# Optimization experiments

Hardware: AMD Instinct MI355X
Metric: run time of the kernel (lower is better)

## Reference

```python
import jax, jax.numpy as jnp
import numpy as np

HIDDEN = 2048
N_HEADS = 16
N_KV_HEADS = 4
HEAD_DIM = 128
N_REP = N_HEADS // N_KV_HEADS
BATCH = 2
SEQ = 2048
SCALE = HEAD_DIM ** -0.5
NEG = -1e9


def apply_rope(x, freqs):
    # x: (b, s, h, d); freqs: (s, d//2) angles. Interleaved-pair rotation.
    cos = jnp.cos(freqs)[None, :, None, :]
    sin = jnp.sin(freqs)[None, :, None, :]
    x1 = x[..., 0::2]
    x2 = x[..., 1::2]
    r1 = x1 * cos - x2 * sin
    r2 = x1 * sin + x2 * cos
    return jnp.stack([r1, r2], axis=-1).reshape(x.shape)


def setup_inputs() -> dict:
    key = jax.random.key(0)
    ks = jax.random.split(key, 6)
    x = jax.random.normal(ks[0], (BATCH, SEQ, HIDDEN), dtype=jnp.float32)
    wq = jax.random.normal(ks[1], (N_HEADS * HEAD_DIM, HIDDEN), dtype=jnp.float32) * 0.02
    wk = jax.random.normal(ks[2], (N_KV_HEADS * HEAD_DIM, HIDDEN), dtype=jnp.float32) * 0.02
    wv = jax.random.normal(ks[3], (N_KV_HEADS * HEAD_DIM, HIDDEN), dtype=jnp.float32) * 0.02
    wo = jax.random.normal(ks[4], (HIDDEN, N_HEADS * HEAD_DIM), dtype=jnp.float32) * 0.02
    # RoPE angle table: pos * theta^{-2i/d}
    inv_freq = 1.0 / (10000.0 ** (jnp.arange(0, HEAD_DIM, 2, dtype=jnp.float32) / HEAD_DIM))
    rope_freqs = jnp.arange(SEQ, dtype=jnp.float32)[:, None] * inv_freq[None, :]  # (S, d/2)
    # additive causal mask
    causal = jnp.tril(jnp.ones((SEQ, SEQ), dtype=bool))
    mask = jnp.where(causal, 0.0, NEG).astype(jnp.float32)[None, None]  # (1,1,S,S)
    return {"x": x, "wq": wq, "wk": wk, "wv": wv, "wo": wo,
            "rope_freqs": rope_freqs, "mask": mask}


def reference(x, wq, wk, wv, wo, rope_freqs, mask):
    b, s, _ = x.shape
    q = (x @ wq.T).reshape(b, s, N_HEADS, HEAD_DIM)
    k = (x @ wk.T).reshape(b, s, N_KV_HEADS, HEAD_DIM)
    v = (x @ wv.T).reshape(b, s, N_KV_HEADS, HEAD_DIM)
    q = apply_rope(q, rope_freqs)
    k = apply_rope(k, rope_freqs)
    new_k, new_v = k, v  # kv cache (no prior cache, start_pos=0)
    # GQA: repeat each kv head n_rep times (matches expand+reshape in source)
    k_rep = jnp.repeat(k, N_REP, axis=2)  # (b, s, n_heads, d)
    v_rep = jnp.repeat(v, N_REP, axis=2)
    scores = jnp.einsum('bqhd,bkhd->bhqk', q, k_rep) * SCALE
    scores = scores + mask
    attn = jax.nn.softmax(scores.astype(jnp.float32), axis=-1).astype(q.dtype)
    out = jnp.einsum('bhqk,bkhd->bqhd', attn, v_rep).reshape(b, s, -1)
    return out @ wo.T, (new_k, new_v)
```

## Files before the change

kernel.cpp:

```cpp
#include <hip/hip_runtime.h>
#include <hip/hip_bf16.h>

#define NH 16
#define NKV 4
#define HD 128
#define QSCALE 0.1275174272f

using bf16x8 = __attribute__((ext_vector_type(8))) __bf16;
using f32x4  = __attribute__((ext_vector_type(4))) float;
using u16x8  = __attribute__((ext_vector_type(8))) unsigned short;
using u16x2  = __attribute__((ext_vector_type(2))) unsigned short;

__device__ __forceinline__ unsigned short f2b(float f) {
  __hip_bfloat16 h = __float2bfloat16(f);
  return __builtin_bit_cast(unsigned short, h);
}
__device__ __forceinline__ float b2f(unsigned short u) {
  unsigned int v = ((unsigned int)u) << 16;
  return __builtin_bit_cast(float, v);
}

__device__ __forceinline__ void glds16(const unsigned short* g, unsigned short* l) {
  __builtin_amdgcn_global_load_lds(
      (const __attribute__((address_space(1))) unsigned int*)(const void*)g,
      (__attribute__((address_space(3))) unsigned int*)(void*)l, 16, 0, 0);
}

__global__ __launch_bounds__(256) void cvt_fused(const float* __restrict__ x,
                                                 const float* __restrict__ wq,
                                                 const float* __restrict__ wk,
                                                 const float* __restrict__ wv,
                                                 const float* __restrict__ wo,
                                                 unsigned short* __restrict__ xb,
                                                 unsigned short* __restrict__ wqkvb,
                                                 unsigned short* __restrict__ wob) {
  int i = blockIdx.x * 256 + threadIdx.x;
  const float* src;
  unsigned short* dst;
  int off;
  if (i < 1048576)      { src = x;  dst = xb;              off = i; }
  else if (i < 1572864) { src = wq; dst = wqkvb;           off = i - 1048576; }
  else if (i < 1703936) { src = wk; dst = wqkvb + 4194304; off = i - 1572864; }
  else if (i < 1835008) { src = wv; dst = wqkvb + 5242880; off = i - 1703936; }
  else                  { src = wo; dst = wob;             off = i - 1835008; }
  const float4* s4 = reinterpret_cast<const float4*>(src) + (size_t)off * 2;
  float4 v0 = s4[0], v1 = s4[1];
  u16x8 o;
  o[0] = f2b(v0.x); o[1] = f2b(v0.y); o[2] = f2b(v0.z); o[3] = f2b(v0.w);
  o[4] = f2b(v1.x); o[5] = f2b(v1.y); o[6] = f2b(v1.z); o[7] = f2b(v1.w);
  reinterpret_cast<u16x8*>(dst)[off] = o;
}

template<int CF32, int WROWS>
__global__ __launch_bounds__(256, 2) void gemm_p(const unsigned short* __restrict__ A,
                                                 const unsigned short* __restrict__ B,
                                                 void* __restrict__ C,
                                                 int N, int K, int nbx) {
  constexpr int AF  = WROWS / 16;
  constexpr int AL  = WROWS / 32;
  constexpr int ACH = WROWS * 8;
  __shared__ unsigned short As[3][ACH * 8];
  __shared__ unsigned short Bs[3][4096];
  const int tid = threadIdx.x, lane = tid & 63, wid = tid >> 6;
  const int wm = wid >> 1, wn = wid & 1;
  const int cpx = gridDim.x >> 3;
  const int wgid = (blockIdx.x & 7) * cpx + (blockIdx.x >> 3);
  const int bx = wgid % nbx, by = wgid / nbx;
  const int row0 = by * (2 * WROWS), col0 = bx * 128;
  const int fr = lane & 15, g = lane >> 4;
  const int NT = K >> 5;

  size_t offA[AL], offB[2];
#pragma unroll
  for (int l = 0; l < AL; l++) {
    int cid = tid + l * 256;
    int R = cid >> 3, p = cid & 7, cl = p ^ (R & 7);
    offA[l] = (size_t)(row0 + 2 * R + (cl >> 2)) * K + (cl & 3) * 8;
  }
#pragma unroll
  for (int l = 0; l < 2; l++) {
    int cid = tid + l * 256;
    int R = cid >> 3, p = cid & 7, cl = p ^ (R & 7);
    offB[l] = (size_t)(col0 + 2 * R + (cl >> 2)) * K + (cl & 3) * 8;
  }

  auto stage = [&](int t, int sb) {
    int k0 = t * 32;
#pragma unroll
    for (int l = 0; l < AL; l++)
      glds16(A + offA[l] + k0, &As[sb][tid * 8 + l * 2048]);
#pragma unroll
    for (int l = 0; l < 2; l++)
      glds16(B + offB[l] + k0, &Bs[sb][tid * 8 + l * 2048]);
  };

  f32x4 acc[AF][4];
#pragma unroll
  for (int i = 0; i < AF; i++)
#pragma unroll
    for (int j = 0; j < 4; j++) acc[i][j] = f32x4{0.f, 0.f, 0.f, 0.f};

  stage(0, 0);
  stage(1, 1);
  if constexpr (WROWS == 128)
    asm volatile("s_waitcnt vmcnt(6)" ::: "memory");
  else
    asm volatile("s_waitcnt vmcnt(4)" ::: "memory");
  __builtin_amdgcn_s_barrier();
  asm volatile("" ::: "memory");

  const int cp8 = ((((fr & 1) << 2) | g) ^ ((fr >> 1) & 7)) * 8;
  const int rr = fr >> 1;

  int rb = 0, sb = 2;
#pragma unroll 1
  for (int t = 0; t < NT; ++t) {
    if (t + 2 < NT) stage(t + 2, sb);

    bf16x8 af[AF], bfr[4];
#pragma unroll
    for (int i = 0; i < AF; i++)
      af[i] = *reinterpret_cast<const bf16x8*>(&As[rb][(wm * (WROWS / 2) + i * 8 + rr) * 64 + cp8]);
#pragma unroll
    for (int j = 0; j < 4; j++)
      bfr[j] = *reinterpret_cast<const bf16x8*>(&Bs[rb][(wn * 32 + j * 8 + rr) * 64 + cp8]);

    __builtin_amdgcn_s_setprio(1);
#pragma unroll
    for (int i = 0; i < AF; i++)
#pragma unroll
      for (int j = 0; j < 4; j++)
        acc[i][j] = __builtin_amdgcn_mfma_f32_16x16x32_bf16(af[i], bfr[j], acc[i][j], 0, 0, 0);
    __builtin_amdgcn_s_setprio(0);

    if (t + 1 < NT) {
      if (t + 2 < NT) {
        if constexpr (WROWS == 128)
          asm volatile("s_waitcnt vmcnt(6)" ::: "memory");
        else
          asm volatile("s_waitcnt vmcnt(4)" ::: "memory");
      } else {
        asm volatile("s_waitcnt vmcnt(0)" ::: "memory");
      }
      __builtin_amdgcn_s_barrier();
      asm volatile("" ::: "memory");
    }
    rb = rb == 2 ? 0 : rb + 1;
    sb = sb == 2 ? 0 : sb + 1;
  }

  const int r4 = g * 4;
#pragma unroll
  for (int i = 0; i < AF; i++) {
#pragma unroll
    for (int j = 0; j < 4; j++) {
      int rbase = row0 + wm * WROWS + i * 16 + r4;
      int cb = col0 + wn * 64 + j * 16 + fr;
#pragma unroll
      for (int r = 0; r < 4; r++) {
        if (CF32)
          reinterpret_cast<float*>(C)[(size_t)(rbase + r) * N + cb] = acc[i][j][r];
        else
          reinterpret_cast<unsigned short*>(C)[(size_t)(rbase + r) * N + cb] = f2b(acc[i][j][r]);
      }
    }
  }
}

__global__ __launch_bounds__(256) void rope_kernel(const unsigned short* __restrict__ qkv,
                                                   const float* __restrict__ freqs,
                                                   unsigned short* __restrict__ qro,
                                                   unsigned short* __restrict__ kro,
                                                   float* __restrict__ newk) {
  const int NQ = 4096 * 16 * 64;
  const int NK = 4096 * 4 * 64;
  int idx = blockIdx.x * 256 + threadIdx.x;
  if (idx >= NQ + NK) return;
  if (idx < NQ) {
    int i = idx & 63;
    int h = (idx >> 6) & 15;
    int row = idx >> 10;
    int s = row & 2047, b = row >> 11;
    float f = freqs[s * 64 + i];
    float c = cosf(f), sn = sinf(f);
    u16x2 xv = *reinterpret_cast<const u16x2*>(qkv + (size_t)row * 3072 + h * 128 + 2 * i);
    float x1 = b2f(xv.x), x2 = b2f(xv.y);
    float r1 = (x1 * c - x2 * sn) * QSCALE;
    float r2 = (x1 * sn + x2 * c) * QSCALE;
    u16x2 o; o.x = f2b(r1); o.y = f2b(r2);
    *reinterpret_cast<u16x2*>(qro + ((size_t)(b * 16 + h) * 2048 + s) * 128 + 2 * i) = o;
  } else {
    idx -= NQ;
    int i = idx & 63;
    int h = (idx >> 6) & 3;
    int row = idx >> 8;
    int s = row & 2047, b = row >> 11;
    float f = freqs[s * 64 + i];
    float c = cosf(f), sn = sinf(f);
    u16x2 xv = *reinterpret_cast<const u16x2*>(qkv + (size_t)row * 3072 + 2048 + h * 128 + 2 * i);
    float x1 = b2f(xv.x), x2 = b2f(xv.y);
    float r1 = x1 * c - x2 * sn;
    float r2 = x1 * sn + x2 * c;
    u16x2 o; o.x = f2b(r1); o.y = f2b(r2);
    *reinterpret_cast<u16x2*>(kro + ((size_t)(b * 4 + h) * 2048 + s) * 128 + 2 * i) = o;
    float2 of; of.x = r1; of.y = r2;
    *reinterpret_cast<float2*>(newk + (size_t)row * 512 + h * 128 + 2 * i) = of;
  }
}

__global__ __launch_bounds__(256) void vtrans_kernel(const unsigned short* __restrict__ qkv,
                                                     unsigned short* __restrict__ vt,
                                                     float* __restrict__ newv) {
  __shared__ unsigned short T[32][136];
  const int st = blockIdx.x;
  const int kvh = blockIdx.y & 3, b = blockIdx.y >> 2;
  const int s0 = st * 32;
  const int t = threadIdx.x;
  const int ls = t >> 3;
  const int ch = (t & 7) * 2;
  const unsigned short* src = qkv + (size_t)(b * 2048 + s0 + ls) * 3072 + 2560 + kvh * 128 + ch * 8;
  u16x8 a0 = *reinterpret_cast<const u16x8*>(src);
  u16x8 a1 = *reinterpret_cast<const u16x8*>(src + 8);
  *reinterpret_cast<u16x8*>(&T[ls][ch * 8])     = a0;
  *reinterpret_cast<u16x8*>(&T[ls][ch * 8 + 8]) = a1;
  float* nv = newv + (size_t)(b * 2048 + s0 + ls) * 512 + kvh * 128 + ch * 8;
  float4 f0, f1, f2, f3;
  f0.x = b2f(a0[0]); f0.y = b2f(a0[1]); f0.z = b2f(a0[2]); f0.w = b2f(a0[3]);
  f1.x = b2f(a0[4]); f1.y = b2f(a0[5]); f1.z = b2f(a0[6]); f1.w = b2f(a0[7]);
  f2.x = b2f(a1[0]); f2.y = b2f(a1[1]); f2.z = b2f(a1[2]); f2.w = b2f(a1[3]);
  f3.x = b2f(a1[4]); f3.y = b2f(a1[5]); f3.z = b2f(a1[6]); f3.w = b2f(a1[7]);
  reinterpret_cast<float4*>(nv)[0] = f0;
  reinterpret_cast<float4*>(nv)[1] = f1;
  reinterpret_cast<float4*>(nv)[2] = f2;
  reinterpret_cast<float4*>(nv)[3] = f3;
  __syncthreads();
  const int d = t >> 1, half = t & 1;
  unsigned short* dst = vt + ((size_t)(b * 4 + kvh) * 128 + d) * 2048 + s0 + half * 16;
  u16x8 o0, o1;
#pragma unroll
  for (int q = 0; q < 8; q++) {
    int slot = half * 16 + q;
    int kl = ((slot >> 2) & 1) * 16 + (slot >> 3) * 4 + (slot & 3);
    o0[q] = T[kl][d];
  }
#pragma unroll
  for (int q = 0; q < 8; q++) {
    int slot = half * 16 + 8 + q;
    int kl = ((slot >> 2) & 1) * 16 + (slot >> 3) * 4 + (slot & 3);
    o1[q] = T[kl][d];
  }
  reinterpret_cast<u16x8*>(dst)[0] = o0;
  reinterpret_cast<u16x8*>(dst)[1] = o1;
}

__global__ __launch_bounds__(256, 4) void attn_kernel(const unsigned short* __restrict__ qro,
                                                      const unsigned short* __restrict__ kro,
                                                      const unsigned short* __restrict__ vt,
                                                      unsigned short* __restrict__ out) {
  __shared__ unsigned short Ks[2][32 * 128];
  __shared__ unsigned short Vs[2][64 * 64];
  const int tid = threadIdx.x, lane = tid & 63, w = tid >> 6;
  const int kvhb = blockIdx.x & 7;
  const int kvh = kvhb & 3, b = kvhb >> 2;
  const int t = 127 - (blockIdx.x >> 3);
  const int h = kvh * 4 + w;
  const int qbase = t * 16;
  const int fr = lane & 15, g = lane >> 4, fk = g * 8;
  const unsigned short* Kp = kro + (size_t)(b * 4 + kvh) * 2048 * 128;
  const unsigned short* Vtp = vt + (size_t)(b * 4 + kvh) * 128 * 2048;
  const unsigned short* Qp = qro + ((size_t)(b * 16 + h) * 2048 + qbase) * 128;

  bf16x8 qf[4];
#pragma unroll
  for (int kk = 0; kk < 4; kk++)
    qf[kk] = *reinterpret_cast<const bf16x8*>(Qp + fr * 128 + kk * 32 + fk);

  u16x8 onesu;
#pragma unroll
  for (int j = 0; j < 8; j++) onesu[j] = 0x3F80;
  bf16x8 ones = __builtin_bit_cast(bf16x8, onesu);

  f32x4 o[8];
#pragma unroll
  for (int dt = 0; dt < 8; dt++) o[dt] = f32x4{0.f, 0.f, 0.f, 0.f};
  f32x4 dacc = f32x4{0.f, 0.f, 0.f, 0.f};
  const int qrow_s = qbase + fr;
  const int nfull = (qbase >= 31) ? ((qbase - 31) >> 5) + 1 : 0;
  const int niter = nfull + 1;

  const int krow = w * 8 + (lane >> 4);
  const int kcol = lane & 15;
  const int vrow = w * 16 + (lane >> 3);
  const int vcol = lane & 7;

  auto stage = [&](int kv0, int buf) {
    unsigned short* Kb = &Ks[buf][0];
    unsigned short* Vb = &Vs[buf][0];
#pragma unroll
    for (int j = 0; j < 2; j++) {
      int r = krow + j * 4;
      glds16(Kp + (size_t)(kv0 + r) * 128 + ((kcol ^ (r & 7)) * 8),
             Kb + (w * 8 + j * 4) * 128);
    }
#pragma unroll
    for (int j = 0; j < 2; j++) {
      int r = vrow + j * 8;
      int u = vcol ^ (r & 7);
      int d = 2 * r + (u >> 2);
      glds16(Vtp + (size_t)d * 2048 + kv0 + (u & 3) * 8,
             Vb + (w * 16 + j * 8) * 64);
    }
  };

  auto step = [&](int kv0, bool mask, int buf) {
    const unsigned short* Kb = &Ks[buf][0];
    const unsigned short* Vb = &Vs[buf][0];
    f32x4 sc[2];
    sc[0] = sc[1] = f32x4{0.f, 0.f, 0.f, 0.f};
    __builtin_amdgcn_s_setprio(1);
#pragma unroll
    for (int kk = 0; kk < 4; kk++) {
      int blk = ((kk * 4 + g) ^ (fr & 7)) * 8;
      bf16x8 ka0 = *reinterpret_cast<const bf16x8*>(Kb + (fr +  0) * 128 + blk);
      bf16x8 ka1 = *reinterpret_cast<const bf16x8*>(Kb + (fr + 16) * 128 + blk);
      sc[0] = __builtin_amdgcn_mfma_f32_16x16x32_bf16(ka0, qf[kk], sc[0], 0, 0, 0);
      sc[1] = __builtin_amdgcn_mfma_f32_16x16x32_bf16(ka1, qf[kk], sc[1], 0, 0, 0);
    }
    __builtin_amdgcn_s_setprio(0);
#pragma unroll
    for (int s = 0; s < 2; s++)
#pragma unroll
      for (int r = 0; r < 4; r++) {
        float v = sc[s][r];
        if (mask && (kv0 + 16 * s + 4 * g + r > qrow_s)) v = -1e30f;
        sc[s][r] = __builtin_amdgcn_exp2f(v);
      }
    u16x8 pau;
#pragma unroll
    for (int j = 0; j < 4; j++) {
      pau[j]     = f2b(sc[0][j]);
      pau[4 + j] = f2b(sc[1][j]);
    }
    bf16x8 pa = __builtin_bit_cast(bf16x8, pau);
    dacc = __builtin_amdgcn_mfma_f32_16x16x32_bf16(pa, ones, dacc, 0, 0, 0);
    __builtin_amdgcn_s_setprio(1);
#pragma unroll
    for (int dt = 0; dt < 8; dt++) {
      int jr = dt * 8 + (fr >> 1);
      int c = ((fr & 1) * 4 + g) ^ (fr >> 1);
      bf16x8 vf = *reinterpret_cast<const bf16x8*>(Vb + jr * 64 + c * 8);
      o[dt] = __builtin_amdgcn_mfma_f32_16x16x32_bf16(pa, vf, o[dt], 0, 0, 0);
    }
    __builtin_amdgcn_s_setprio(0);
  };

  stage(0, 0);
  int buf = 0;
  for (int i = 0; i < niter; i++) {
    __syncthreads();
    if (i + 1 < niter) stage((i + 1) * 32, buf ^ 1);
    step(i * 32, i == nfull, buf);
    buf ^= 1;
  }

#pragma unroll
  for (int r = 0; r < 4; r++) {
    float inv = 1.0f / dacc[r];
    int qrow = qbase + g * 4 + r;
    size_t rowoff = ((size_t)b * 2048 + qrow) * 2048 + (size_t)h * 128;
#pragma unroll
    for (int dt = 0; dt < 8; dt++)
      out[rowoff + dt * 16 + fr] = f2b(o[dt][r] * inv);
  }
}

extern "C" void kernel_launch(void* const* d_in, const int* in_sizes, int n_in,
                              void* d_out, int out_size, void* d_ws, size_t ws_size,
                              hipStream_t stream) {
  const float* x  = (const float*)d_in[0];
  const float* wq = (const float*)d_in[1];
  const float* wk = (const float*)d_in[2];
  const float* wv = (const float*)d_in[3];
  const float* wo = (const float*)d_in[4];
  const float* freqs = (const float*)d_in[5];

  char* ws = (char*)d_ws;
  unsigned short* xb    = (unsigned short*)(ws);
  unsigned short* attn  = xb;
  unsigned short* wqkvb = (unsigned short*)(ws + 16777216);
  unsigned short* wob   = (unsigned short*)(ws + 29360128);
  unsigned short* qkv   = (unsigned short*)(ws + 37748736);
  unsigned short* qro   = (unsigned short*)(ws + 62914560);
  unsigned short* kro   = (unsigned short*)(ws + 79691776);
  unsigned short* vt    = (unsigned short*)(ws + 83886080);

  float* out_o = (float*)d_out;
  float* out_k = (float*)d_out + 8388608;
  float* out_v = (float*)d_out + 10485760;

  cvt_fused<<<9216, 256, 0, stream>>>(x, wq, wk, wv, wo, xb, wqkvb, wob);

  gemm_p<0, 128><<<384, 256, 0, stream>>>(xb, wqkvb, qkv, 3072, 2048, 24);

  rope_kernel<<<20480, 256, 0, stream>>>(qkv, freqs, qro, kro, out_k);
  vtrans_kernel<<<dim3(64, 8), 256, 0, stream>>>(qkv, vt, out_v);

  attn_kernel<<<1024, 256, 0, stream>>>(qro, kro, vt, attn);

  gemm_p<1, 64><<<512, 256, 0, stream>>>(attn, wob, out_o, 2048, 2048, 16);
}
```

Baseline: 216.5 us.

## Replace GEMM with 8-wave 128x256 tile kernel using split-phase staging

Swaps the 4-wave GEMM for an 8-wave, 512-thread kernel with 128x256 output tiles and a K-step of 64. Each iteration is split into two halves, and the global-to-LDS staging for a future tile is interleaved with the MFMA work through explicit barriers and sched_barriers. The aim is more operand reuse per tile and better overlap of memory traffic with matrix math. In exchange it uses more LDS and registers, allows one block per CU, and leaves fewer blocks for the output projection (256), which risks lower occupancy and tail effects.

```diff
diff --git a/kernel.cpp b/kernel.cpp
--- a/kernel.cpp
+++ b/kernel.cpp
@@ -51,110 +51,127 @@
   reinterpret_cast<u16x8*>(dst)[off] = o;
 }
 
-template<int CF32, int WROWS>
-__global__ __launch_bounds__(256, 2) void gemm_p(const unsigned short* __restrict__ A,
-                                                 const unsigned short* __restrict__ B,
-                                                 void* __restrict__ C,
-                                                 int N, int K, int nbx) {
-  constexpr int AF  = WROWS / 16;
-  constexpr int AL  = WROWS / 32;
-  constexpr int ACH = WROWS * 8;
-  __shared__ unsigned short As[3][ACH * 8];
-  __shared__ unsigned short Bs[3][4096];
-  const int tid = threadIdx.x, lane = tid & 63, wid = tid >> 6;
-  const int wm = wid >> 1, wn = wid & 1;
+template<int CF32>
+__global__ __launch_bounds__(512, 1) void gemm8(const unsigned short* __restrict__ A,
+                                                const unsigned short* __restrict__ B,
+                                                void* __restrict__ C,
+                                                int N, int K, int nbx) {
+  __shared__ unsigned short As[3][128 * 64];
+  __shared__ unsigned short Bs[3][256 * 64];
+  const int tid = threadIdx.x, lane = tid & 63;
+  const int wid = tid >> 6, wm = wid >> 2, wn = wid & 3;
   const int cpx = gridDim.x >> 3;
   const int wgid = (blockIdx.x & 7) * cpx + (blockIdx.x >> 3);
   const int bx = wgid % nbx, by = wgid / nbx;
-  const int row0 = by * (2 * WROWS), col0 = bx * 128;
+  const int row0 = by * 128, col0 = bx * 256;
   const int fr = lane & 15, g = lane >> 4;
-  const int NT = K >> 5;
-
-  size_t offA[AL], offB[2];
-#pragma unroll
-  for (int l = 0; l < AL; l++) {
-    int cid = tid + l * 256;
-    int R = cid >> 3, p = cid & 7, cl = p ^ (R & 7);
-    offA[l] = (size_t)(row0 + 2 * R + (cl >> 2)) * K + (cl & 3) * 8;
-  }
+  const int NT = K >> 6;
+
+  size_t offA[2], offB[4];
 #pragma unroll
   for (int l = 0; l < 2; l++) {
-    int cid = tid + l * 256;
-    int R = cid >> 3, p = cid & 7, cl = p ^ (R & 7);
-    offB[l] = (size_t)(col0 + 2 * R + (cl >> 2)) * K + (cl & 3) * 8;
-  }
-
-  auto stage = [&](int t, int sb) {
-    int k0 = t * 32;
-#pragma unroll
-    for (int l = 0; l < AL; l++)
-      glds16(A + offA[l] + k0, &As[sb][tid * 8 + l * 2048]);
-#pragma unroll
-    for (int l = 0; l < 2; l++)
-      glds16(B + offB[l] + k0, &Bs[sb][tid * 8 + l * 2048]);
-  };
-
-  f32x4 acc[AF][4];
-#pragma unroll
-  for (int i = 0; i < AF; i++)
+    int cid = tid + l * 512, R = cid >> 3, phys = cid & 7, cl = phys ^ (R & 7);
+    offA[l] = (size_t)(row0 + R) * K + cl * 8;
+  }
+#pragma unroll
+  for (int l = 0; l < 4; l++) {
+    int cid = tid + l * 512, R = cid >> 3, phys = cid & 7, cl = phys ^ (R & 7);
+    offB[l] = (size_t)(col0 + R) * K + cl * 8;
+  }
+
+  auto stage0 = [&](int t, int sb) {
+    int k0 = t * 64;
+    glds16(A + offA[0] + k0, &As[sb][tid * 8]);
+    glds16(A + offA[1] + k0, &As[sb][(tid + 512) * 8]);
+    glds16(B + offB[0] + k0, &Bs[sb][tid * 8]);
+  };
+  auto stage1 = [&](int t, int sb) {
+    int k0 = t * 64;
+    glds16(B + offB[1] + k0, &Bs[sb][(tid + 512) * 8]);
+    glds16(B + offB[2] + k0, &Bs[sb][(tid + 1024) * 8]);
+    glds16(B + offB[3] + k0, &Bs[sb][(tid + 1536) * 8]);
+  };
+
+  const int ca = fr & 7;
+  auto ldA = [&](int rb, int mf, int ks) {
+    return *reinterpret_cast<const bf16x8*>(
+        &As[rb][(wm * 64 + mf * 16 + fr) * 64 + (((ks << 2) | g) ^ ca) * 8]);
+  };
+  auto ldB = [&](int rb, int nf, int ks) {
+    return *reinterpret_cast<const bf16x8*>(
+        &Bs[rb][(wn * 64 + nf * 16 + fr) * 64 + (((ks << 2) | g) ^ ca) * 8]);
+  };
+
+  f32x4 acc[4][4];
+#pragma unroll
+  for (int i = 0; i < 4; i++)
 #pragma unroll
     for (int j = 0; j < 4; j++) acc[i][j] = f32x4{0.f, 0.f, 0.f, 0.f};
 
-  stage(0, 0);
-  stage(1, 1);
-  if constexpr (WROWS == 128)
-    asm volatile("s_waitcnt vmcnt(6)" ::: "memory");
-  else
-    asm volatile("s_waitcnt vmcnt(4)" ::: "memory");
+  stage0(0, 0); stage1(0, 0);
+  stage0(1, 1); stage1(1, 1);
+  asm volatile("s_waitcnt vmcnt(6)" ::: "memory");
   __builtin_amdgcn_s_barrier();
-  asm volatile("" ::: "memory");
-
-  const int cp8 = ((((fr & 1) << 2) | g) ^ ((fr >> 1) & 7)) * 8;
-  const int rr = fr >> 1;
+  __builtin_amdgcn_sched_barrier(0);
 
   int rb = 0, sb = 2;
 #pragma unroll 1
   for (int t = 0; t < NT; ++t) {
-    if (t + 2 < NT) stage(t + 2, sb);
-
-    bf16x8 af[AF], bfr[4];
-#pragma unroll
-    for (int i = 0; i < AF; i++)
-      af[i] = *reinterpret_cast<const bf16x8*>(&As[rb][(wm * (WROWS / 2) + i * 8 + rr) * 64 + cp8]);
-#pragma unroll
-    for (int j = 0; j < 4; j++)
-      bfr[j] = *reinterpret_cast<const bf16x8*>(&Bs[rb][(wn * 32 + j * 8 + rr) * 64 + cp8]);
-
+    bf16x8 bfr[4][2];
+#pragma unroll
+    for (int nf = 0; nf < 4; nf++) { bfr[nf][0] = ldB(rb, nf, 0); bfr[nf][1] = ldB(rb, nf, 1); }
+    bf16x8 a0[2][2];
+#pragma unroll
+    for (int mf = 0; mf < 2; mf++) { a0[mf][0] = ldA(rb, mf, 0); a0[mf][1] = ldA(rb, mf, 1); }
+    if (t + 2 < NT) stage0(t + 2, sb);
+    __builtin_amdgcn_s_barrier();
+    asm volatile("s_waitcnt lgkmcnt(0)" ::: "memory");
+    __builtin_amdgcn_sched_barrier(0);
     __builtin_amdgcn_s_setprio(1);
 #pragma unroll
-    for (int i = 0; i < AF; i++)
-#pragma unroll
-      for (int j = 0; j < 4; j++)
-        acc[i][j] = __builtin_amdgcn_mfma_f32_16x16x32_bf16(af[i], bfr[j], acc[i][j], 0, 0, 0);
+    for (int mf = 0; mf < 2; mf++)
+#pragma unroll
+      for (int nf = 0; nf < 4; nf++) {
+        acc[mf][nf] = __builtin_amdgcn_mfma_f32_16x16x32_bf16(a0[mf][0], bfr[nf][0], acc[mf][nf], 0, 0, 0);
+        acc[mf][nf] = __builtin_amdgcn_mfma_f32_16x16x32_bf16(a0[mf][1], bfr[nf][1], acc[mf][nf], 0, 0, 0);
+      }
     __builtin_amdgcn_s_setprio(0);
+    __builtin_amdgcn_sched_barrier(0);
+    __builtin_amdgcn_s_barrier();
+
+    bf16x8 a1[2][2];
+#pragma unroll
+    for (int mf = 0; mf < 2; mf++) { a1[mf][0] = ldA(rb, mf + 2, 0); a1[mf][1] = ldA(rb, mf + 2, 1); }
+    if (t + 2 < NT) stage1(t + 2, sb);
+    __builtin_amdgcn_s_barrier();
+    asm volatile("s_waitcnt lgkmcnt(0)" ::: "memory");
+    __builtin_amdgcn_sched_barrier(0);
+    __builtin_amdgcn_s_setprio(1);
+#pragma unroll
+    for (int mf = 0; mf < 2; mf++)
+#pragma unroll
+      for (int nf = 0; nf < 4; nf++) {
+        acc[mf + 2][nf] = __builtin_amdgcn_mfma_f32_16x16x32_bf16(a1[mf][0], bfr[nf][0], acc[mf + 2][nf], 0, 0, 0);
+        acc[mf + 2][nf] = __builtin_amdgcn_mfma_f32_16x16x32_bf16(a1[mf][1], bfr[nf][1], acc[mf + 2][nf], 0, 0, 0);
+      }
+    __builtin_amdgcn_s_setprio(0);
+    __builtin_amdgcn_sched_barrier(0);
 
     if (t + 1 < NT) {
-      if (t + 2 < NT) {
-        if constexpr (WROWS == 128)
-          asm volatile("s_waitcnt vmcnt(6)" ::: "memory");
-        else
-          asm volatile("s_waitcnt vmcnt(4)" ::: "memory");
-      } else {
-        asm volatile("s_waitcnt vmcnt(0)" ::: "memory");
-      }
+      if (t + 2 < NT) asm volatile("s_waitcnt vmcnt(6)" ::: "memory");
+      else            asm volatile("s_waitcnt vmcnt(0)" ::: "memory");
       __builtin_amdgcn_s_barrier();
-      asm volatile("" ::: "memory");
+      __builtin_amdgcn_sched_barrier(0);
     }
     rb = rb == 2 ? 0 : rb + 1;
     sb = sb == 2 ? 0 : sb + 1;
   }
 
-  const int r4 = g * 4;
-#pragma unroll
-  for (int i = 0; i < AF; i++) {
+#pragma unroll
+  for (int i = 0; i < 4; i++) {
 #pragma unroll
     for (int j = 0; j < 4; j++) {
-      int rbase = row0 + wm * WROWS + i * 16 + r4;
+      int rbase = row0 + wm * 64 + i * 16 + g * 4;
       int cb = col0 + wn * 64 + j * 16 + fr;
 #pragma unroll
       for (int r = 0; r < 4; r++) {
@@ -400,12 +417,12 @@
 
   cvt_fused<<<9216, 256, 0, stream>>>(x, wq, wk, wv, wo, xb, wqkvb, wob);
 
-  gemm_p<0, 128><<<384, 256, 0, stream>>>(xb, wqkvb, qkv, 3072, 2048, 24);
+  gemm8<0><<<384, 512, 0, stream>>>(xb, wqkvb, qkv, 3072, 2048, 12);
 
   rope_kernel<<<20480, 256, 0, stream>>>(qkv, freqs, qro, kro, out_k);
   vtrans_kernel<<<dim3(64, 8), 256, 0, stream>>>(qkv, vt, out_v);
 
   attn_kernel<<<1024, 256, 0, stream>>>(qro, kro, vt, attn);
 
-  gemm_p<1, 64><<<512, 256, 0, stream>>>(attn, wob, out_o, 2048, 2048, 16);
-}
+  gemm8<1><<<256, 512, 0, stream>>>(attn, wob, out_o, 2048, 2048, 8);
+}
```

After: 212.1 us. 2.0% less time.

## Replace 3-stage GEMM with templated double-buffered fat-tile GEMM

Applied to the files above, without the earlier changes.

Replaces the GEMM kernel with a templated version that has configurable block tiles and warp layouts. It uses two LDS buffers with a __syncthreads per K step instead of three buffers with explicit vmcnt waits. The QKV projection now uses 128x256 tiles with a 1x4 warp grid, and the output projection uses 256x128 tiles with a 4x1 warp grid and half as many blocks. The larger tiles aim for more reuse per block, but the shallower pipeline and full barrier each step can expose load latency. There is also a risk of launch/grid mismatch or register pressure under launch_bounds(256,3).

```diff
diff --git a/kernel.cpp b/kernel.cpp
--- a/kernel.cpp
+++ b/kernel.cpp
@@ -51,36 +51,34 @@
   reinterpret_cast<u16x8*>(dst)[off] = o;
 }
 
-template<int CF32, int WROWS>
-__global__ __launch_bounds__(256, 2) void gemm_p(const unsigned short* __restrict__ A,
-                                                 const unsigned short* __restrict__ B,
-                                                 void* __restrict__ C,
-                                                 int N, int K, int nbx) {
-  constexpr int AF  = WROWS / 16;
-  constexpr int AL  = WROWS / 32;
-  constexpr int ACH = WROWS * 8;
-  __shared__ unsigned short As[3][ACH * 8];
-  __shared__ unsigned short Bs[3][4096];
-  const int tid = threadIdx.x, lane = tid & 63, wid = tid >> 6;
-  const int wm = wid >> 1, wn = wid & 1;
+template<int CF32, int BM, int BN, int NWM, int NWN>
+__global__ __launch_bounds__(256, 3) void gemm_fat(const unsigned short* __restrict__ A,
+                                                   const unsigned short* __restrict__ B,
+                                                   void* __restrict__ C,
+                                                   int N, int K, int nbx) {
+  constexpr int WM = BM / NWM, WN = BN / NWN;
+  constexpr int AF = WM / 16, BF = WN / 16;
+  constexpr int AL = BM / 64, BL = BN / 64;
+  __shared__ unsigned short As[2][BM * 32];
+  __shared__ unsigned short Bs[2][BN * 32];
+  const int tid = threadIdx.x, lane = tid & 63;
+  const int wid = tid >> 6, wm = wid / NWN, wn = wid % NWN;
   const int cpx = gridDim.x >> 3;
   const int wgid = (blockIdx.x & 7) * cpx + (blockIdx.x >> 3);
   const int bx = wgid % nbx, by = wgid / nbx;
-  const int row0 = by * (2 * WROWS), col0 = bx * 128;
+  const int row0 = by * BM, col0 = bx * BN;
   const int fr = lane & 15, g = lane >> 4;
   const int NT = K >> 5;
 
-  size_t offA[AL], offB[2];
+  size_t offA[AL], offB[BL];
 #pragma unroll
   for (int l = 0; l < AL; l++) {
-    int cid = tid + l * 256;
-    int R = cid >> 3, p = cid & 7, cl = p ^ (R & 7);
+    int cid = tid + l * 256, R = cid >> 3, phys = cid & 7, cl = phys ^ (R & 7);
     offA[l] = (size_t)(row0 + 2 * R + (cl >> 2)) * K + (cl & 3) * 8;
   }
 #pragma unroll
-  for (int l = 0; l < 2; l++) {
-    int cid = tid + l * 256;
-    int R = cid >> 3, p = cid & 7, cl = p ^ (R & 7);
+  for (int l = 0; l < BL; l++) {
+    int cid = tid + l * 256, R = cid >> 3, phys = cid & 7, cl = phys ^ (R & 7);
     offB[l] = (size_t)(col0 + 2 * R + (cl >> 2)) * K + (cl & 3) * 8;
   }
 
@@ -88,74 +86,51 @@
     int k0 = t * 32;
 #pragma unroll
     for (int l = 0; l < AL; l++)
-      glds16(A + offA[l] + k0, &As[sb][tid * 8 + l * 2048]);
-#pragma unroll
-    for (int l = 0; l < 2; l++)
-      glds16(B + offB[l] + k0, &Bs[sb][tid * 8 + l * 2048]);
+      glds16(A + offA[l] + k0, &As[sb][(tid + l * 256) * 8]);
+#pragma unroll
+    for (int l = 0; l < BL; l++)
+      glds16(B + offB[l] + k0, &Bs[sb][(tid + l * 256) * 8]);
   };
 
-  f32x4 acc[AF][4];
+  auto ldfrag = [&](const unsigned short* buf, int row) {
+    int R = row >> 1;
+    int phys = ((((row & 1) << 2) | g) ^ (R & 7));
+    return *reinterpret_cast<const bf16x8*>(&buf[R * 64 + phys * 8]);
+  };
+
+  f32x4 acc[AF][BF];
 #pragma unroll
   for (int i = 0; i < AF; i++)
 #pragma unroll
-    for (int j = 0; j < 4; j++) acc[i][j] = f32x4{0.f, 0.f, 0.f, 0.f};
+    for (int j = 0; j < BF; j++) acc[i][j] = f32x4{0.f, 0.f, 0.f, 0.f};
 
   stage(0, 0);
-  stage(1, 1);
-  if constexpr (WROWS == 128)
-    asm volatile("s_waitcnt vmcnt(6)" ::: "memory");
-  else
-    asm volatile("s_waitcnt vmcnt(4)" ::: "memory");
-  __builtin_amdgcn_s_barrier();
-  asm volatile("" ::: "memory");
-
-  const int cp8 = ((((fr & 1) << 2) | g) ^ ((fr >> 1) & 7)) * 8;
-  const int rr = fr >> 1;
-
-  int rb = 0, sb = 2;
+  int buf = 0;
 #pragma unroll 1
   for (int t = 0; t < NT; ++t) {
-    if (t + 2 < NT) stage(t + 2, sb);
-
-    bf16x8 af[AF], bfr[4];
-#pragma unroll
-    for (int i = 0; i < AF; i++)
-      af[i] = *reinterpret_cast<const bf16x8*>(&As[rb][(wm * (WROWS / 2) + i * 8 + rr) * 64 + cp8]);
-#pragma unroll
-    for (int j = 0; j < 4; j++)
-      bfr[j] = *reinterpret_cast<const bf16x8*>(&Bs[rb][(wn * 32 + j * 8 + rr) * 64 + cp8]);
-
+    __syncthreads();
+    if (t + 1 < NT) stage(t + 1, buf ^ 1);
+    bf16x8 af[AF], bfr[BF];
+#pragma unroll
+    for (int mf = 0; mf < AF; mf++) af[mf] = ldfrag(As[buf], wm * WM + mf * 16 + fr);
+#pragma unroll
+    for (int nf = 0; nf < BF; nf++) bfr[nf] = ldfrag(Bs[buf], wn * WN + nf * 16 + fr);
     __builtin_amdgcn_s_setprio(1);
 #pragma unroll
-    for (int i = 0; i < AF; i++)
-#pragma unroll
-      for (int j = 0; j < 4; j++)
-        acc[i][j] = __builtin_amdgcn_mfma_f32_16x16x32_bf16(af[i], bfr[j], acc[i][j], 0, 0, 0);
+    for (int mf = 0; mf < AF; mf++)
+#pragma unroll
+      for (int nf = 0; nf < BF; nf++)
+        acc[mf][nf] = __builtin_amdgcn_mfma_f32_16x16x32_bf16(af[mf], bfr[nf], acc[mf][nf], 0, 0, 0);
     __builtin_amdgcn_s_setprio(0);
-
-    if (t + 1 < NT) {
-      if (t + 2 < NT) {
-        if constexpr (WROWS == 128)
-          asm volatile("s_waitcnt vmcnt(6)" ::: "memory");
-        else
-          asm volatile("s_waitcnt vmcnt(4)" ::: "memory");
-      } else {
-        asm volatile("s_waitcnt vmcnt(0)" ::: "memory");
-      }
-      __builtin_amdgcn_s_barrier();
-      asm volatile("" ::: "memory");
-    }
-    rb = rb == 2 ? 0 : rb + 1;
-    sb = sb == 2 ? 0 : sb + 1;
-  }
-
-  const int r4 = g * 4;
+    buf ^= 1;
+  }
+
 #pragma unroll
   for (int i = 0; i < AF; i++) {
 #pragma unroll
-    for (int j = 0; j < 4; j++) {
-      int rbase = row0 + wm * WROWS + i * 16 + r4;
-      int cb = col0 + wn * 64 + j * 16 + fr;
+    for (int j = 0; j < BF; j++) {
+      int rbase = row0 + wm * WM + i * 16 + g * 4;
+      int cb = col0 + wn * WN + j * 16 + fr;
 #pragma unroll
       for (int r = 0; r < 4; r++) {
         if (CF32)
@@ -400,12 +375,12 @@
 
   cvt_fused<<<9216, 256, 0, stream>>>(x, wq, wk, wv, wo, xb, wqkvb, wob);
 
-  gemm_p<0, 128><<<384, 256, 0, stream>>>(xb, wqkvb, qkv, 3072, 2048, 24);
+  gemm_fat<0, 128, 256, 1, 4><<<384, 256, 0, stream>>>(xb, wqkvb, qkv, 3072, 2048, 12);
 
   rope_kernel<<<20480, 256, 0, stream>>>(qkv, freqs, qro, kro, out_k);
   vtrans_kernel<<<dim3(64, 8), 256, 0, stream>>>(qkv, vt, out_v);
 
   attn_kernel<<<1024, 256, 0, stream>>>(qro, kro, vt, attn);
 
-  gemm_p<1, 64><<<512, 256, 0, stream>>>(attn, wob, out_o, 2048, 2048, 16);
-}
+  gemm_fat<1, 256, 128, 4, 1><<<256, 256, 0, stream>>>(attn, wob, out_o, 2048, 2048, 16);
+}
```

After: 440.8 us. 104% more time.
